# Kernel tuning notes

Measured on AMD Instinct MI355X. Metric: run time of the kernel, lower is better.

Reference implementation:

```python
import jax, jax.numpy as jnp
import numpy as np

STRIDES = (4, 8, 16, 32)
OUT = 7
RATIO = 2  # sampling_ratio per bin dim (ROIAlignV2)
P = OUT * RATIO  # sample points per spatial dim


def _bilinear_axis(coord, size):
    # ROIAlign semantics: zero contribution outside [-1, size], clamp into [0, size-1]
    valid = ((coord > -1.0) & (coord < size)).astype(coord.dtype)
    c = jnp.clip(coord, 0.0, size - 1)
    i0 = jnp.floor(c).astype(jnp.int32)
    i1 = jnp.minimum(i0 + 1, size - 1)
    frac = c - i0.astype(coord.dtype)
    return i0, i1, (1.0 - frac) * valid, frac * valid


def _roi_align(fmap, bidx, boxes, stride):
    """ROIAlignV2 (aligned=True, sampling_ratio=2). fmap: [B,H,W,C], boxes: [N,4] in image coords."""
    H, W = fmap.shape[1], fmap.shape[2]
    x1 = boxes[:, 0] / stride - 0.5
    y1 = boxes[:, 1] / stride - 0.5
    x2 = boxes[:, 2] / stride - 0.5
    y2 = boxes[:, 3] / stride - 0.5
    steps = (jnp.arange(P, dtype=fmap.dtype) + 0.5) / P  # [P] uniform sample centers
    px = x1[:, None] + (x2 - x1)[:, None] * steps  # [N,P]
    py = y1[:, None] + (y2 - y1)[:, None] * steps  # [N,P]
    ix0, ix1, wx0, wx1 = _bilinear_axis(px, W)
    iy0, iy1, wy0, wy1 = _bilinear_axis(py, H)
    b = bidx[:, None, None]

    def g(yi, xi):
        return fmap[b, yi[:, :, None], xi[:, None, :]]  # [N,P,P,C]

    val = ((wy0[:, :, None] * wx0[:, None, :])[..., None] * g(iy0, ix0)
           + (wy0[:, :, None] * wx1[:, None, :])[..., None] * g(iy0, ix1)
           + (wy1[:, :, None] * wx0[:, None, :])[..., None] * g(iy1, ix0)
           + (wy1[:, :, None] * wx1[:, None, :])[..., None] * g(iy1, ix1))
    N, C = boxes.shape[0], fmap.shape[3]
    pooled = val.reshape(N, OUT, RATIO, OUT, RATIO, C).mean(axis=(2, 4))  # avg within each bin
    return pooled.transpose(0, 3, 1, 2).reshape(N, C * OUT * OUT)  # torch [N,C,7,7].flatten(1)


def _head(fms, rois, fc1_w, fc1_b, fc2_w, fc2_b, p_w, p_b):
    bidx = rois[:, 0].astype(jnp.int32)
    boxes = rois[:, 1:5]
    w = boxes[:, 2] - boxes[:, 0]
    h = boxes[:, 3] - boxes[:, 1]
    # standard FPN level assignment: k = floor(4 + log2(sqrt(area)/224)), clamp [2,5]
    k = jnp.floor(4.0 + jnp.log2(jnp.sqrt(jnp.maximum(w * h, 1e-6)) / 224.0))
    lvl = jnp.clip(k, 2.0, 5.0).astype(jnp.int32) - 2  # 0->stride4 ... 3->stride32
    pooled = jnp.stack([_roi_align(fm.transpose(0, 2, 3, 1), bidx, boxes, s)
                        for fm, s in zip(fms, STRIDES)])  # [4,N,D]
    pool5 = pooled[lvl, jnp.arange(rois.shape[0])]  # [N,D] select per-roi level
    fc1 = jax.nn.relu(pool5 @ fc1_w.T + fc1_b)
    fc2 = jax.nn.relu(fc1 @ fc2_w.T + fc2_b)
    return fc2 @ p_w.T + p_b  # prob: [N, 5*n*nheads]


def setup_inputs():
    key = jax.random.key(0)
    ks = jax.random.split(key, 12)
    B, C = 2, 256
    ImH, ImW = 768, 1280
    N = 1024
    NUM_CLASSES, NHEADS = 2, 2
    D = C * OUT * OUT
    fms = [jax.random.normal(ks[i], (B, C, ImH // s, ImW // s), dtype=jnp.float32)
           for i, s in enumerate(STRIDES)]
    # boxes with log-uniform sizes in [32, 512] px, clipped to image
    wh = jnp.exp(jax.random.uniform(ks[4], (N, 2), minval=float(np.log(32.0)), maxval=float(np.log(512.0))))
    cxy = jax.random.uniform(ks[5], (N, 2)) * jnp.array([ImW, ImH], jnp.float32)
    x1 = jnp.clip(cxy[:, 0] - wh[:, 0] / 2, 0.0, ImW - 2.0)
    y1 = jnp.clip(cxy[:, 1] - wh[:, 1] / 2, 0.0, ImH - 2.0)
    x2 = jnp.clip(cxy[:, 0] + wh[:, 0] / 2, x1 + 1.0, ImW - 1.0)
    y2 = jnp.clip(cxy[:, 1] + wh[:, 1] / 2, y1 + 1.0, ImH - 1.0)
    bidx = jax.random.randint(ks[6], (N,), 0, B).astype(jnp.float32)
    rois = jnp.stack([bidx, x1, y1, x2, y2], axis=1)
    fc1_w = jax.random.normal(ks[7], (1024, D), dtype=jnp.float32) / np.sqrt(D).astype(np.float32)
    fc1_b = jnp.zeros((1024,), jnp.float32)
    fc2_w = jax.random.normal(ks[8], (1024, 1024), dtype=jnp.float32) / 32.0
    fc2_b = jnp.zeros((1024,), jnp.float32)
    p_w = jax.random.normal(ks[9], (5 * NUM_CLASSES * NHEADS, 1024), dtype=jnp.float32) / 32.0
    p_b = jnp.zeros((5 * NUM_CLASSES * NHEADS,), jnp.float32)
    return {"fm0": fms[0], "fm1": fms[1], "fm2": fms[2], "fm3": fms[3], "rois": rois,
            "fc1_w": fc1_w, "fc1_b": fc1_b, "fc2_w": fc2_w, "fc2_b": fc2_b,
            "p_w": p_w, "p_b": p_b}


def reference(fm0, fm1, fm2, fm3, rois, fc1_w, fc1_b, fc2_w, fc2_b, p_w, p_b):
    return _head((fm0, fm1, fm2, fm3), rois, fc1_w, fc1_b, fc2_w, fc2_b, p_w, p_b)
```

## Files before the change

kernel.cpp:

```cpp
#include <hip/hip_runtime.h>
#include <hip/hip_bf16.h>
#include <cstddef>
#include <cstdint>


#define NROIS 1024
#define C_CH  256
#define OUTP  7
#define DFEAT (C_CH * OUTP * OUTP)
#define HID   1024
#define NCLS  20

__device__ __forceinline__ unsigned short f2bf(float x) {
    union { float f; uint32_t u; } v; v.f = x;
    uint32_t r = v.u + 0x7fffu + ((v.u >> 16) & 1u);
    return (unsigned short)(r >> 16);
}
__device__ __forceinline__ float bf2f(unsigned short h) {
    union { uint32_t u; float f; } v; v.u = ((uint32_t)h) << 16;
    return v.f;
}

__device__ __forceinline__ void g2lds16(const void* g, void* l) {
    __builtin_amdgcn_global_load_lds(
        (const __attribute__((address_space(1))) void*)g,
        (__attribute__((address_space(3))) void*)l,
        16, 0, 0);
}

typedef __attribute__((ext_vector_type(8))) short bf16x8;
typedef __attribute__((ext_vector_type(4))) float f32x4;

__global__ __launch_bounds__(256) void roi_pool_split(
    const float* __restrict__ fm0, const float* __restrict__ fm1,
    const float* __restrict__ fm2, const float* __restrict__ fm3,
    const float* __restrict__ rois,
    unsigned short* __restrict__ ph, unsigned short* __restrict__ pl)
{
    const int roi = blockIdx.x;
    const int t   = threadIdx.x;

    __shared__ float s_box[5];
    __shared__ int   s_ix0[16], s_ix1[16], s_iy0[16], s_iy1[16];
    __shared__ float s_wx0[16], s_wx1[16], s_wy0[16], s_wy1[16];

    if (t < 5) s_box[t] = rois[(size_t)roi * 5 + t];
    __syncthreads();

    const int   b   = (int)s_box[0];
    const float bx1 = s_box[1], by1 = s_box[2], bx2 = s_box[3], by2 = s_box[4];

    const float w = bx2 - bx1, h = by2 - by1;
    float kf = floorf(4.0f + log2f(sqrtf(fmaxf(w * h, 1e-6f)) / 224.0f));
    kf = fminf(fmaxf(kf, 2.0f), 5.0f);
    const int lvl    = (int)kf - 2;
    const int stride = 4 << lvl;
    const int H  = 768  / stride;
    const int Wd = 1280 / stride;
    const float* fm = (lvl == 0) ? fm0 : (lvl == 1) ? fm1 : (lvl == 2) ? fm2 : fm3;

    if (t < 14) {
        const float x1s = bx1 / (float)stride - 0.5f;
        const float x2s = bx2 / (float)stride - 0.5f;
        const float coord = x1s + (x2s - x1s) * (((float)t + 0.5f) / 14.0f);
        const float valid = (coord > -1.0f && coord < (float)Wd) ? 1.0f : 0.0f;
        const float cc = fminf(fmaxf(coord, 0.0f), (float)(Wd - 1));
        const int i0 = (int)floorf(cc);
        s_ix0[t] = i0; s_ix1[t] = min(i0 + 1, Wd - 1);
        const float fr = cc - (float)i0;
        s_wx0[t] = (1.0f - fr) * valid; s_wx1[t] = fr * valid;
    } else if (t >= 16 && t < 30) {
        const int j = t - 16;
        const float y1s = by1 / (float)stride - 0.5f;
        const float y2s = by2 / (float)stride - 0.5f;
        const float coord = y1s + (y2s - y1s) * (((float)j + 0.5f) / 14.0f);
        const float valid = (coord > -1.0f && coord < (float)H) ? 1.0f : 0.0f;
        const float cc = fminf(fmaxf(coord, 0.0f), (float)(H - 1));
        const int i0 = (int)floorf(cc);
        s_iy0[j] = i0; s_iy1[j] = min(i0 + 1, H - 1);
        const float fr = cc - (float)i0;
        s_wy0[j] = (1.0f - fr) * valid; s_wy1[j] = fr * valid;
    }
    __syncthreads();

    const int wv = t >> 6, lane = t & 63;
    const int jx = lane & 15, grp = lane >> 4;
    const int xj = min(jx, 13);
    const int x0 = s_ix0[xj], x1 = s_ix1[xj];
    const float wx0 = s_wx0[xj], wx1 = s_wx1[xj];
    const bool xact = (jx < 14);

    const size_t hw = (size_t)H * Wd;
    const float* fmb = fm + (size_t)b * C_CH * hw;

    for (int ci = 0; ci < 64; ++ci) {
        const int c = wv * 64 + ci;
        const float* fb = fmb + (size_t)c * hw;
        #pragma unroll
        for (int ky = 0; ky < 4; ++ky) {
            const int jy = ky * 4 + grp;
            const int yj = min(jy, 13);
            const int y0 = s_iy0[yj], y1 = s_iy1[yj];
            const float a0 = s_wy0[yj], a1 = s_wy1[yj];
            const float* r0 = fb + (size_t)y0 * Wd;
            const float* r1 = fb + (size_t)y1 * Wd;
            float v = a0 * (wx0 * r0[x0] + wx1 * r0[x1])
                    + a1 * (wx0 * r1[x0] + wx1 * r1[x1]);
            if (!xact || jy >= 14) v = 0.0f;
            v += __shfl_down(v, 1);
            v += __shfl_down(v, 16);
            if (((grp & 1) == 0) && ((jx & 1) == 0) && jx < 14) {
                const int by = ky * 2 + (grp >> 1);
                if (by < 7) {
                    const int bx = jx >> 1;
                    const float r = v * 0.25f;
                    const size_t d = (size_t)roi * DFEAT + c * 49 + by * 7 + bx;
                    const unsigned short hh = f2bf(r);
                    ph[d] = hh;
                    pl[d] = f2bf(r - bf2f(hh));
                }
            }
        }
    }
}

__global__ __launch_bounds__(256) void split_fp32_bf16(
    const float* __restrict__ w, unsigned short* __restrict__ h,
    unsigned short* __restrict__ l, int n4)
{
    int i = blockIdx.x * 256 + threadIdx.x;
    const int stride = gridDim.x * 256;
    for (; i < n4; i += stride) {
        const float4 v = *(const float4*)(w + (size_t)i * 4);
        ushort4 hh, ll;
        hh.x = f2bf(v.x); ll.x = f2bf(v.x - bf2f(hh.x));
        hh.y = f2bf(v.y); ll.y = f2bf(v.y - bf2f(hh.y));
        hh.z = f2bf(v.z); ll.z = f2bf(v.z - bf2f(hh.z));
        hh.w = f2bf(v.w); ll.w = f2bf(v.w - bf2f(hh.w));
        *(ushort4*)(h + (size_t)i * 4) = hh;
        *(ushort4*)(l + (size_t)i * 4) = ll;
    }
}

#define GBM 128
#define GBN 128
#define GBK 32

__global__ __launch_bounds__(256) void gemm_bf16x3(
    const unsigned short* __restrict__ Ah, const unsigned short* __restrict__ Al,
    const unsigned short* __restrict__ Bh, const unsigned short* __restrict__ Bl,
    float* __restrict__ part, int K, int ksplit)
{
    __shared__ __align__(16) unsigned short sAh[GBM * GBK];
    __shared__ __align__(16) unsigned short sAl[GBM * GBK];
    __shared__ __align__(16) unsigned short sBh[GBN * GBK];
    __shared__ __align__(16) unsigned short sBl[GBN * GBK];

    const int t  = threadIdx.x;
    const int bm = blockIdx.y * GBM, bn = blockIdx.x * GBN;
    const int k0 = blockIdx.z * ksplit, k1 = k0 + ksplit;
    const int lane = t & 63, wv = t >> 6;
    const int wr = wv >> 1, wc = wv & 1;
    const int lm = lane & 15, quad = lane >> 4;

    f32x4 acc[4][4] = {};

    const int srow = t >> 2;
    const int skc  = (t & 3) * 8;

    for (int kk = k0; kk < k1; kk += GBK) {
        #pragma unroll
        for (int q = 0; q < 2; ++q) {
            const int row = q * 64 + srow;
            const size_t ga = (size_t)(bm + row) * K + kk + skc;
            const size_t gb = (size_t)(bn + row) * K + kk + skc;
            const int lo = q * 4096 + t * 16;
            g2lds16(Ah + ga, (char*)sAh + lo);
            g2lds16(Al + ga, (char*)sAl + lo);
            g2lds16(Bh + gb, (char*)sBh + lo);
            g2lds16(Bl + gb, (char*)sBl + lo);
        }
        __syncthreads();

        bf16x8 fah[4], fal[4], fbh[4], fbl[4];
        #pragma unroll
        for (int i = 0; i < 4; ++i) {
            fah[i] = *(const bf16x8*)&sAh[(wr * 64 + i * 16 + lm) * GBK + quad * 8];
            fal[i] = *(const bf16x8*)&sAl[(wr * 64 + i * 16 + lm) * GBK + quad * 8];
            fbh[i] = *(const bf16x8*)&sBh[(wc * 64 + i * 16 + lm) * GBK + quad * 8];
            fbl[i] = *(const bf16x8*)&sBl[(wc * 64 + i * 16 + lm) * GBK + quad * 8];
        }
        #pragma unroll
        for (int i = 0; i < 4; ++i)
            #pragma unroll
            for (int j = 0; j < 4; ++j)
                acc[i][j] = __builtin_amdgcn_mfma_f32_16x16x32_bf16(fah[i], fbh[j], acc[i][j], 0, 0, 0);
        #pragma unroll
        for (int i = 0; i < 4; ++i)
            #pragma unroll
            for (int j = 0; j < 4; ++j)
                acc[i][j] = __builtin_amdgcn_mfma_f32_16x16x32_bf16(fah[i], fbl[j], acc[i][j], 0, 0, 0);
        #pragma unroll
        for (int i = 0; i < 4; ++i)
            #pragma unroll
            for (int j = 0; j < 4; ++j)
                acc[i][j] = __builtin_amdgcn_mfma_f32_16x16x32_bf16(fal[i], fbh[j], acc[i][j], 0, 0, 0);
        __syncthreads();
    }

    float* out = part + (size_t)blockIdx.z * (HID * NROIS);
    #pragma unroll
    for (int i = 0; i < 4; ++i) {
        const int mbase = bm + wr * 64 + i * 16 + quad * 4;
        #pragma unroll
        for (int j = 0; j < 4; ++j) {
            const int n = bn + wc * 64 + j * 16 + lm;
            #pragma unroll
            for (int r = 0; r < 4; ++r)
                out[(size_t)(mbase + r) * HID + n] = acc[i][j][r];
        }
    }
}

__global__ __launch_bounds__(256) void reduce_bias_relu(
    const float* __restrict__ part, const float* __restrict__ bias,
    int S, int mode, unsigned short* __restrict__ oh,
    unsigned short* __restrict__ ol, float* __restrict__ ofp)
{
    const int i4 = blockIdx.x * 256 + threadIdx.x;
    const size_t off = (size_t)i4 * 4;
    const int n = (int)(off & (HID - 1));
    float4 s = *(const float4*)(part + off);
    for (int z = 1; z < S; ++z) {
        const float4 p = *(const float4*)(part + (size_t)z * HID * NROIS + off);
        s.x += p.x; s.y += p.y; s.z += p.z; s.w += p.w;
    }
    const float4 b = *(const float4*)(bias + n);
    s.x = fmaxf(s.x + b.x, 0.0f);
    s.y = fmaxf(s.y + b.y, 0.0f);
    s.z = fmaxf(s.z + b.z, 0.0f);
    s.w = fmaxf(s.w + b.w, 0.0f);
    if (mode == 0) {
        *(float4*)(ofp + off) = s;
    } else {
        ushort4 hh, ll;
        hh.x = f2bf(s.x); ll.x = f2bf(s.x - bf2f(hh.x));
        hh.y = f2bf(s.y); ll.y = f2bf(s.y - bf2f(hh.y));
        hh.z = f2bf(s.z); ll.z = f2bf(s.z - bf2f(hh.z));
        hh.w = f2bf(s.w); ll.w = f2bf(s.w - bf2f(hh.w));
        *(ushort4*)(oh + off) = hh;
        *(ushort4*)(ol + off) = ll;
    }
}

__global__ __launch_bounds__(256) void pred_kernel(
    const float* __restrict__ A, const float* __restrict__ Wm,
    const float* __restrict__ bias, float* __restrict__ out)
{
    const int i = blockIdx.x;
    const int t = threadIdx.x;
    const int j = t & 31;
    const int s = t >> 5;

    __shared__ float red[8][32];

    float acc = 0.0f;
    if (j < NCLS) {
        const float4* a4 = (const float4*)(A  + (size_t)i * HID + s * 128);
        const float4* w4 = (const float4*)(Wm + (size_t)j * HID + s * 128);
        #pragma unroll 8
        for (int q = 0; q < 32; ++q) {
            const float4 a = a4[q], w = w4[q];
            acc += a.x * w.x + a.y * w.y + a.z * w.z + a.w * w.w;
        }
    }
    red[s][j] = acc;
    __syncthreads();
    if (s == 0 && j < NCLS) {
        float v = bias[j];
        #pragma unroll
        for (int q = 0; q < 8; ++q) v += red[q][j];
        out[(size_t)i * NCLS + j] = v;
    }
}

extern "C" void kernel_launch(void* const* d_in, const int* in_sizes, int n_in,
                              void* d_out, int out_size, void* d_ws, size_t ws_size,
                              hipStream_t stream) {
    (void)in_sizes; (void)n_in; (void)out_size;

    const float* fm0   = (const float*)d_in[0];
    const float* fm1   = (const float*)d_in[1];
    const float* fm2   = (const float*)d_in[2];
    const float* fm3   = (const float*)d_in[3];
    const float* rois  = (const float*)d_in[4];
    const float* fc1_w = (const float*)d_in[5];
    const float* fc1_b = (const float*)d_in[6];
    const float* fc2_w = (const float*)d_in[7];
    const float* fc2_b = (const float*)d_in[8];
    const float* p_w   = (const float*)d_in[9];
    const float* p_b   = (const float*)d_in[10];

    const size_t SZ_POOL = (size_t)NROIS * DFEAT * 2;
    const size_t SZ_W1   = (size_t)HID * DFEAT * 2;
    const size_t SZ_W2   = (size_t)HID * HID * 2;
    const size_t SZ_FC1  = (size_t)NROIS * HID * 2;
    const size_t SZ_FC2O = (size_t)NROIS * HID * 4;
    const size_t SZ_PART1 = (size_t)HID * NROIS * 4;

    const size_t fixed = 2 * SZ_POOL + 2 * SZ_W1 + 2 * SZ_W2 + 2 * SZ_FC1 + SZ_FC2O;
    int S1 = 8;
    while (S1 > 1 && fixed + (size_t)S1 * SZ_PART1 > ws_size) S1 >>= 1;
    const int S2 = (S1 < 4) ? S1 : 4;

    char* p = (char*)d_ws;
    unsigned short* ph   = (unsigned short*)p; p += SZ_POOL;
    unsigned short* pl   = (unsigned short*)p; p += SZ_POOL;
    unsigned short* w1h  = (unsigned short*)p; p += SZ_W1;
    unsigned short* w1l  = (unsigned short*)p; p += SZ_W1;
    unsigned short* w2h  = (unsigned short*)p; p += SZ_W2;
    unsigned short* w2l  = (unsigned short*)p; p += SZ_W2;
    unsigned short* fc1h = (unsigned short*)p; p += SZ_FC1;
    unsigned short* fc1l = (unsigned short*)p; p += SZ_FC1;
    float* fc2o = (float*)p; p += SZ_FC2O;
    float* part = (float*)p;

    float* outp = (float*)d_out;

    split_fp32_bf16<<<4096, 256, 0, stream>>>(fc1_w, w1h, w1l, HID * DFEAT / 4);
    split_fp32_bf16<<<1024, 256, 0, stream>>>(fc2_w, w2h, w2l, HID * HID / 4);

    roi_pool_split<<<NROIS, 256, 0, stream>>>(fm0, fm1, fm2, fm3, rois, ph, pl);

    {
        dim3 grid(HID / GBN, NROIS / GBM, S1);
        gemm_bf16x3<<<grid, 256, 0, stream>>>(ph, pl, w1h, w1l, part, DFEAT, DFEAT / S1);
    }
    reduce_bias_relu<<<NROIS * HID / 4 / 256, 256, 0, stream>>>(
        part, fc1_b, S1, 1, fc1h, fc1l, (float*)nullptr);

    {
        dim3 grid(HID / GBN, NROIS / GBM, S2);
        gemm_bf16x3<<<grid, 256, 0, stream>>>(fc1h, fc1l, w2h, w2l, part, HID, HID / S2);
    }
    reduce_bias_relu<<<NROIS * HID / 4 / 256, 256, 0, stream>>>(
        part, fc2_b, S2, 0, (unsigned short*)nullptr, (unsigned short*)nullptr, fc2o);

    pred_kernel<<<NROIS, 256, 0, stream>>>(fc2o, p_w, p_b, outp);
}
```

Measured before the change: 548.6 us.

## Stage ROI footprint in LDS per channel and split channels across blocks

The ROI-align kernel now copies each channel's bounding-box footprint of the feature map into shared memory with row-coalesced loads. It then computes the 196 bilinear samples from LDS with precomputed offsets and weights, and averages them into the 49 bins. Channels are split across a second grid dimension to double the block count. This is meant to replace scattered global gathers with contiguous loads and on-chip reuse. The cost is two block-wide barriers per channel and a fixed LDS footprint capacity that could be exceeded by very large boxes.

```diff
diff --git a/kernel.cpp b/kernel.cpp
--- a/kernel.cpp
+++ b/kernel.cpp
@@ -11,6 +11,8 @@
 #define HID   1024
 #define NCLS  20
 
+#define FP_CAP 1152
+
 __device__ __forceinline__ unsigned short f2bf(float x) {
     union { float f; uint32_t u; } v; v.f = x;
     uint32_t r = v.u + 0x7fffu + ((v.u >> 16) & 1u);
@@ -31,7 +33,7 @@
 typedef __attribute__((ext_vector_type(8))) short bf16x8;
 typedef __attribute__((ext_vector_type(4))) float f32x4;
 
-__global__ __launch_bounds__(256) void roi_pool_split(
+__global__ __launch_bounds__(256) void roi_pool_lds(
     const float* __restrict__ fm0, const float* __restrict__ fm1,
     const float* __restrict__ fm2, const float* __restrict__ fm3,
     const float* __restrict__ rois,
@@ -43,6 +45,8 @@
     __shared__ float s_box[5];
     __shared__ int   s_ix0[16], s_ix1[16], s_iy0[16], s_iy1[16];
     __shared__ float s_wx0[16], s_wx1[16], s_wy0[16], s_wy1[16];
+    __shared__ __align__(16) float s_fp[4][FP_CAP];
+    __shared__ __align__(16) float s_samp[4][200];
 
     if (t < 5) s_box[t] = rois[(size_t)roi * 5 + t];
     __syncthreads();
@@ -83,44 +87,87 @@
     }
     __syncthreads();
 
+    const int xmin = s_ix0[0], xmax = s_ix1[13];
+    const int ymin = s_iy0[0], ymax = s_iy1[13];
+    const int rowlen = xmax - xmin + 1;
+    const int rows   = ymax - ymin + 1;
+
     const int wv = t >> 6, lane = t & 63;
-    const int jx = lane & 15, grp = lane >> 4;
-    const int xj = min(jx, 13);
-    const int x0 = s_ix0[xj], x1 = s_ix1[xj];
-    const float wx0 = s_wx0[xj], wx1 = s_wx1[xj];
-    const bool xact = (jx < 14);
+    float* fpw   = s_fp[wv];
+    float* sampw = s_samp[wv];
+
+    int   a00[4], a01[4], a10[4], a11[4];
+    float w00[4], w01[4], w10[4], w11[4];
+    bool  sval[4];
+    #pragma unroll
+    for (int j = 0; j < 4; ++j) {
+        const int s = j * 64 + lane;
+        const bool v = (s < 196);
+        sval[j] = v;
+        const int ss = v ? s : 0;
+        const int jy = ss / 14;
+        const int jx = ss - jy * 14;
+        const int ro0 = (s_iy0[jy] - ymin) * rowlen;
+        const int ro1 = (s_iy1[jy] - ymin) * rowlen;
+        const int lx0 = s_ix0[jx] - xmin;
+        const int lx1 = s_ix1[jx] - xmin;
+        a00[j] = ro0 + lx0; a01[j] = ro0 + lx1;
+        a10[j] = ro1 + lx0; a11[j] = ro1 + lx1;
+        const float wy0 = s_wy0[jy], wy1 = s_wy1[jy];
+        const float wx0 = s_wx0[jx], wx1 = s_wx1[jx];
+        w00[j] = wy0 * wx0; w01[j] = wy0 * wx1;
+        w10[j] = wy1 * wx0; w11[j] = wy1 * wx1;
+    }
+
+    const int bin = lane;
+    const int by = bin / 7, bx = bin - by * 7;
+    const int s00 = 28 * by + 2 * bx;
+    const bool bact = (bin < 49);
+
+    const int lpr_sh = (rowlen > 16) ? 5 : (rowlen > 8 ? 4 : 3);
+    const int lpr = 1 << lpr_sh;
+    const int rpi = 64 >> lpr_sh;
+    const int rlane = lane >> lpr_sh;
+    const int clane = lane & (lpr - 1);
 
     const size_t hw = (size_t)H * Wd;
     const float* fmb = fm + (size_t)b * C_CH * hw;
-
-    for (int ci = 0; ci < 64; ++ci) {
-        const int c = wv * 64 + ci;
-        const float* fb = fmb + (size_t)c * hw;
-        #pragma unroll
-        for (int ky = 0; ky < 4; ++ky) {
-            const int jy = ky * 4 + grp;
-            const int yj = min(jy, 13);
-            const int y0 = s_iy0[yj], y1 = s_iy1[yj];
-            const float a0 = s_wy0[yj], a1 = s_wy1[yj];
-            const float* r0 = fb + (size_t)y0 * Wd;
-            const float* r1 = fb + (size_t)y1 * Wd;
-            float v = a0 * (wx0 * r0[x0] + wx1 * r0[x1])
-                    + a1 * (wx0 * r1[x0] + wx1 * r1[x1]);
-            if (!xact || jy >= 14) v = 0.0f;
-            v += __shfl_down(v, 1);
-            v += __shfl_down(v, 16);
-            if (((grp & 1) == 0) && ((jx & 1) == 0) && jx < 14) {
-                const int by = ky * 2 + (grp >> 1);
-                if (by < 7) {
-                    const int bx = jx >> 1;
-                    const float r = v * 0.25f;
-                    const size_t d = (size_t)roi * DFEAT + c * 49 + by * 7 + bx;
-                    const unsigned short hh = f2bf(r);
-                    ph[d] = hh;
-                    pl[d] = f2bf(r - bf2f(hh));
-                }
+    const int c0w = blockIdx.y * 128 + wv * 32;
+
+    size_t obase = (size_t)roi * DFEAT + (size_t)c0w * 49 + bin;
+
+    for (int ci = 0; ci < 32; ++ci) {
+        const int c = c0w + ci;
+        const float* fb = fmb + (size_t)c * hw + (size_t)ymin * Wd + xmin;
+
+        for (int r = 0; r < rows; r += rpi) {
+            const int rr = r + rlane;
+            const bool rok = (rr < rows);
+            const float* gsrc = fb + (size_t)rr * Wd;
+            float* ldst = fpw + rr * rowlen;
+            for (int cc0 = 0; cc0 < rowlen; cc0 += lpr) {
+                const int cc = cc0 + clane;
+                if (rok && cc < rowlen) ldst[cc] = gsrc[cc];
             }
         }
+        __syncthreads();
+
+        #pragma unroll
+        for (int j = 0; j < 4; ++j) {
+            const float v = w00[j] * fpw[a00[j]] + w01[j] * fpw[a01[j]]
+                          + w10[j] * fpw[a10[j]] + w11[j] * fpw[a11[j]];
+            if (sval[j]) sampw[j * 64 + lane] = v;
+        }
+        __syncthreads();
+
+        if (bact) {
+            const float r = 0.25f * (sampw[s00] + sampw[s00 + 1]
+                                   + sampw[s00 + 14] + sampw[s00 + 15]);
+            const unsigned short hh = f2bf(r);
+            ph[obase] = hh;
+            pl[obase] = f2bf(r - bf2f(hh));
+        }
+        obase += 49;
     }
 }
 
@@ -330,7 +377,7 @@
     split_fp32_bf16<<<4096, 256, 0, stream>>>(fc1_w, w1h, w1l, HID * DFEAT / 4);
     split_fp32_bf16<<<1024, 256, 0, stream>>>(fc2_w, w2h, w2l, HID * HID / 4);
 
-    roi_pool_split<<<NROIS, 256, 0, stream>>>(fm0, fm1, fm2, fm3, rois, ph, pl);
+    roi_pool_lds<<<dim3(NROIS, 2), 256, 0, stream>>>(fm0, fm1, fm2, fm3, rois, ph, pl);
 
     {
         dim3 grid(HID / GBN, NROIS / GBM, S1);
```

Result: slower. 753.3 us (+37.3%).
